# Performance work log

Hardware: AMD Instinct MI355X
Metric: run time of the kernel (lower is better)

The kernel has to match this reference:

```python
import jax, jax.numpy as jnp
import numpy as np

B = 65536
D_EMB = 512      # embedding_dim
D_SPD = 1        # speed_dim
D_LAT = 128      # speed_latent_dim
H = 256          # hidden_size
K = 6            # num_branch
D_IN = D_EMB + D_LAT  # 640, branch/speed-head input dim


def _lin(key, din, dout):
    kw, kb = jax.random.split(key)
    W = jax.random.normal(kw, (din, dout), dtype=jnp.float32) * 0.02
    b = jax.random.normal(kb, (dout,), dtype=jnp.float32) * 0.02
    return W, b


def setup_inputs() -> dict:
    key = jax.random.key(0)
    ks = jax.random.split(key, 16)
    embedding = jax.random.normal(ks[0], (B, D_EMB), dtype=jnp.float32)
    speed = jax.random.uniform(ks[1], (B, D_SPD), dtype=jnp.float32)
    command = jax.random.randint(ks[2], (B,), 1, K + 1, dtype=jnp.int32)  # values 1..6
    # speed input MLP: speed_dim -> H -> D_LAT
    Wsi1, bsi1 = _lin(ks[3], D_SPD, H)
    Wsi2, bsi2 = _lin(ks[4], H, D_LAT)
    # speed prediction head: D_IN -> H -> H -> speed_dim
    Wso1, bso1 = _lin(ks[5], D_IN, H)
    Wso2, bso2 = _lin(ks[6], H, H)
    Wso3, bso3 = _lin(ks[7], H, D_SPD)
    # K branch heads, stacked on leading axis: D_IN -> H -> H -> 3, sigmoid
    def _stack(key, din, dout):
        kw, kb = jax.random.split(key)
        W = jax.random.normal(kw, (K, din, dout), dtype=jnp.float32) * 0.02
        b = jax.random.normal(kb, (K, dout), dtype=jnp.float32) * 0.02
        return W, b
    Wb1, bb1 = _stack(ks[8], D_IN, H)
    Wb2, bb2 = _stack(ks[9], H, H)
    Wb3, bb3 = _stack(ks[10], H, 3)
    return dict(embedding=embedding, speed=speed, command=command,
                Wsi1=Wsi1, bsi1=bsi1, Wsi2=Wsi2, bsi2=bsi2,
                Wso1=Wso1, bso1=bso1, Wso2=Wso2, bso2=bso2, Wso3=Wso3, bso3=bso3,
                Wb1=Wb1, bb1=bb1, Wb2=Wb2, bb2=bb2, Wb3=Wb3, bb3=bb3)


def reference(embedding, speed, command,
              Wsi1, bsi1, Wsi2, bsi2,
              Wso1, bso1, Wso2, bso2, Wso3, bso3,
              Wb1, bb1, Wb2, bb2, Wb3, bb3):
    # speed -> latent
    sp = jax.nn.relu(speed @ Wsi1 + bsi1) @ Wsi2 + bsi2          # [B, D_LAT]
    emb = jnp.concatenate([embedding, sp], axis=1)               # [B, D_IN]
    # compute ALL K branch heads (as the original does), then mask by command
    h = jax.nn.relu(jnp.einsum('bd,kdh->bkh', emb, Wb1) + bb1)   # [B, K, H]
    h = jax.nn.relu(jnp.einsum('bkh,khj->bkj', h, Wb2) + bb2)    # [B, K, H]
    ctrl_all = jax.nn.sigmoid(jnp.einsum('bkh,kho->bko', h, Wb3) + bb3)  # [B, K, 3]
    mask = (command[:, None] - 1 == jnp.arange(K)[None, :]).astype(ctrl_all.dtype)  # [B, K]
    control_pred = jnp.sum(ctrl_all * mask[:, :, None], axis=1)  # [B, 3]
    # speed prediction head
    hs = jax.nn.relu(emb @ Wso1 + bso1)
    hs = jax.nn.relu(hs @ Wso2 + bso2)
    speed_pred = hs @ Wso3 + bso3                                # [B, 1]
    return control_pred, speed_pred
```

## Files before the change

kernel.cpp:

```cpp
#include <hip/hip_runtime.h>
#include <hip/hip_bf16.h>


#define NB 65536
#define NBRB 1030

typedef __attribute__((ext_vector_type(8))) short short8;
typedef __attribute__((ext_vector_type(4))) float f32x4;
typedef unsigned short bhalf;
typedef unsigned int u32;

__device__ __forceinline__ bhalf f2b(float x) {
    __hip_bfloat16 h = __float2bfloat16(x);
    return *reinterpret_cast<bhalf*>(&h);
}
__device__ __forceinline__ void gll16(const void* g, void* l) {
    __builtin_amdgcn_global_load_lds(
        (const __attribute__((address_space(1))) u32*)g,
        (__attribute__((address_space(3))) u32*)l, 16, 0, 0);
}
__device__ __forceinline__ int sadr(int row, int cb) {
    return row * 64 + (cb ^ (((row >> 1) & 3) << 4));
}
__device__ __forceinline__ int yadr(int row, int cb) {
    return row * 512 + (cb ^ ((row & 7) << 4));
}
__device__ __forceinline__ void wvm6() { asm volatile("s_waitcnt vmcnt(6)" ::: "memory"); }
__device__ __forceinline__ void wvm0() { asm volatile("s_waitcnt vmcnt(0)" ::: "memory"); }
__device__ __forceinline__ void wlgkm0() { asm volatile("s_waitcnt lgkmcnt(0)" ::: "memory"); }

__global__ __launch_bounds__(256) void k_wprep(
    const float* __restrict__ Wsi2, const float* __restrict__ Wso1,
    const float* __restrict__ Wso2, const float* __restrict__ Wb1,
    const float* __restrict__ Wb2,
    bhalf* __restrict__ Wsi2T, bhalf* __restrict__ Wso1T,
    bhalf* __restrict__ Wso2T, bhalf* __restrict__ Wb1T,
    bhalf* __restrict__ Wb2T) {
    __shared__ float T[64][65];
    const int id = blockIdx.x, t = threadIdx.x;
    const float* src; bhalf* dst; int K, N, tk, tn, b;
    if (id < 8)        { src = Wsi2; dst = Wsi2T; K = 256; N = 128; b = 0; int tl = id;      tk = tl / 2; tn = tl % 2; }
    else if (id < 48)  { src = Wso1; dst = Wso1T; K = 640; N = 256; b = 0; int tl = id - 8;  tk = tl / 4; tn = tl % 4; }
    else if (id < 64)  { src = Wso2; dst = Wso2T; K = 256; N = 256; b = 0; int tl = id - 48; tk = tl / 4; tn = tl % 4; }
    else if (id < 304) { src = Wb1;  dst = Wb1T;  K = 640; N = 256; int li = id - 64;  b = li / 40; int tl = li % 40; tk = tl / 4; tn = tl % 4; }
    else               { src = Wb2;  dst = Wb2T;  K = 256; N = 256; int li = id - 304; b = li / 16; int tl = li % 16; tk = tl / 4; tn = tl % 4; }
    const int k0 = tk * 64, n0 = tn * 64;
    src += (size_t)b * K * N; dst += (size_t)b * N * K;
    const int c = t & 63, r0 = t >> 6;
#pragma unroll
    for (int j = 0; j < 16; ++j) {
        int r = r0 + j * 4;
        T[r][c] = src[(size_t)(k0 + r) * N + n0 + c];
    }
    __syncthreads();
#pragma unroll
    for (int j = 0; j < 16; ++j) {
        int r = r0 + j * 4;
        dst[(size_t)(n0 + r) * K + k0 + c] = f2b(T[c][r]);
    }
}

__global__ __launch_bounds__(256) void k_prep(
    const float* __restrict__ speed, const float* __restrict__ Wsi1,
    const float* __restrict__ bsi1, const bhalf* __restrict__ Wsi2T,
    const float* __restrict__ bsi2, const int* __restrict__ cmd,
    bhalf* __restrict__ spb, int* __restrict__ bcnt) {
    __shared__ bhalf A[64 * 72];
    __shared__ bhalf BT[128 * 72];
    const int t = threadIdx.x, lane = t & 63, wid = t >> 6;
    const int rbase = blockIdx.x * 64;
    if (wid == 0) {
        int c = cmd[rbase + lane] - 1;
        int v = 0;
#pragma unroll
        for (int g = 0; g < 6; ++g) {
            unsigned long long m = __ballot(c == g);
            if (lane == g) v = (int)__popcll(m);
        }
        if (lane < 6) bcnt[blockIdx.x * 6 + lane] = v;
    }
    const int wm = wid >> 1, wn = wid & 1;
    f32x4 acc[2][4];
    for (int m = 0; m < 2; ++m) for (int n = 0; n < 4; ++n)
        for (int r = 0; r < 4; ++r) acc[m][n][r] = 0.f;
    const int ar = t >> 2, kp = (t & 3) * 16;
    const float s = speed[rbase + ar];
    for (int kc = 0; kc < 4; ++kc) {
        short8 w0, w1;
#pragma unroll
        for (int j = 0; j < 8; ++j) {
            int k = kc * 64 + kp + j;
            w0[j] = (short)f2b(fmaxf(fmaf(s, Wsi1[k], bsi1[k]), 0.f));
            w1[j] = (short)f2b(fmaxf(fmaf(s, Wsi1[k + 8], bsi1[k + 8]), 0.f));
        }
        *(short8*)&A[ar * 72 + kp] = w0;
        *(short8*)&A[ar * 72 + kp + 8] = w1;
#pragma unroll
        for (int j = 0; j < 4; ++j) {
            int ch = t + j * 256;
            int n2 = ch >> 3, ko = (ch & 7) * 8;
            *(short8*)&BT[n2 * 72 + ko] =
                *(const short8*)(Wsi2T + n2 * 256 + kc * 64 + ko);
        }
        __syncthreads();
#pragma unroll
        for (int ks = 0; ks < 2; ++ks) {
            short8 a[2], b[4];
#pragma unroll
            for (int m = 0; m < 2; ++m)
                a[m] = *(const short8*)&A[(wm * 32 + m * 16 + (lane & 15)) * 72 + ks * 32 + (lane >> 4) * 8];
#pragma unroll
            for (int n = 0; n < 4; ++n)
                b[n] = *(const short8*)&BT[(wn * 64 + n * 16 + (lane & 15)) * 72 + ks * 32 + (lane >> 4) * 8];
#pragma unroll
            for (int m = 0; m < 2; ++m)
#pragma unroll
                for (int n = 0; n < 4; ++n)
                    acc[m][n] = __builtin_amdgcn_mfma_f32_16x16x32_bf16(a[m], b[n], acc[m][n], 0, 0, 0);
        }
        __syncthreads();
    }
#pragma unroll
    for (int m = 0; m < 2; ++m)
#pragma unroll
    for (int n = 0; n < 4; ++n) {
        int col = wn * 64 + n * 16 + (lane & 15);
        float bias = bsi2[col];
#pragma unroll
        for (int r = 0; r < 4; ++r) {
            int row = rbase + wm * 32 + m * 16 + (lane >> 4) * 4 + r;
            spb[row * 128 + col] = f2b(acc[m][n][r] + bias);
        }
    }
}

__global__ __launch_bounds__(1024) void k_scan(
    const int* __restrict__ bcnt, int* __restrict__ chunkoff,
    int* __restrict__ pad) {
    __shared__ int sc[1024];
    __shared__ int tot[8];
    __shared__ int spo[8];
    const int t = threadIdx.x;
    for (int g = 0; g < 6; ++g) {
        int v = bcnt[t * 6 + g];
        sc[t] = v;
        __syncthreads();
        for (int s = 1; s < 1024; s <<= 1) {
            int u = (t >= s) ? sc[t - s] : 0;
            __syncthreads();
            sc[t] += u;
            __syncthreads();
        }
        if (t == 1023) tot[g] = sc[t];
        chunkoff[t * 6 + g] = sc[t] - v;
        __syncthreads();
    }
    if (t == 0) {
        int off = 0;
        for (int g = 0; g < 6; ++g) {
            spo[g] = off; pad[g] = off; pad[8 + g] = tot[g];
            off += ((tot[g] + 63) >> 6) << 6;
        }
        spo[6] = off; pad[6] = off;
    }
    __syncthreads();
    for (int g = 0; g < 6; ++g) chunkoff[t * 6 + g] += spo[g];
}

__global__ __launch_bounds__(256) void k_scatter(
    const int* __restrict__ cmd, const int* __restrict__ chunkoff,
    int* __restrict__ perm) {
    const int lane = threadIdx.x & 63, w = threadIdx.x >> 6;
    const int chunk = blockIdx.x * 4 + w;
    const int idx = chunk * 64 + lane;
    const int c = cmd[idx] - 1;
#pragma unroll
    for (int g = 0; g < 6; ++g) {
        unsigned long long m = __ballot(c == g);
        if (c == g) {
            int pos = chunkoff[chunk * 6 + g] + (int)__popcll(m & ((1ull << lane) - 1ull));
            perm[pos] = idx;
        }
    }
}

__global__ __launch_bounds__(256, 3) void k_head(
    const float* __restrict__ emb, const bhalf* __restrict__ spb,
    const bhalf* __restrict__ Wso1T, const float* __restrict__ bso1,
    const bhalf* __restrict__ Wso2T, const float* __restrict__ bso2,
    const float* __restrict__ Wso3, const float* __restrict__ bso3,
    const bhalf* __restrict__ Wb1T, const float* __restrict__ bb1,
    const bhalf* __restrict__ Wb2T, const float* __restrict__ bb2,
    const float* __restrict__ Wb3, const float* __restrict__ bb3,
    const int* __restrict__ pad, const int* __restrict__ perm,
    float* __restrict__ out) {
    __shared__ __align__(16) char L[49152];
    char* const SB0 = L;
    char* const SAr = L + 32768;
    char* const Yb  = L;
    const int t = threadIdx.x, lane = t & 63, wid = t >> 6;
    const bool isB = blockIdx.x < NBRB;
    int tstart, DOUT, gcnt, gbase;
    const bhalf *W1T, *W2T; const float *b1, *b2, *W3, *b3;
    if (isB) {
        tstart = blockIdx.x * 64;
        if (tstart >= pad[6]) return;
        int g = 0;
        while (pad[g + 1] <= tstart) ++g;
        gbase = pad[g]; gcnt = pad[8 + g];
        W1T = Wb1T + (size_t)g * (256 * 640); b1 = bb1 + g * 256;
        W2T = Wb2T + (size_t)g * (256 * 256); b2 = bb2 + g * 256;
        W3  = Wb3  + (size_t)g * (256 * 3);   b3 = bb3 + g * 3;
        DOUT = 3;
    } else {
        tstart = (blockIdx.x - NBRB) * 64;
        gbase = 0; gcnt = NB;
        W1T = Wso1T; b1 = bso1; W2T = Wso2T; b2 = bso2; W3 = Wso3; b3 = bso3;
        DOUT = 1;
    }

    const int rowA0 = t >> 3, rowA1 = rowA0 + 32, rowS = t >> 2;
    int ra0, ra1, raS;
    if (isB) {
        int p0 = tstart + rowA0, p1 = tstart + rowA1, pS = tstart + rowS;
        ra0 = ((p0 - gbase) < gcnt) ? perm[p0] : 0;
        ra1 = ((p1 - gbase) < gcnt) ? perm[p1] : 0;
        raS = ((pS - gbase) < gcnt) ? perm[pS] : 0;
    } else {
        ra0 = tstart + rowA0; ra1 = tstart + rowA1; raS = tstart + rowS;
    }
    const int lcA0 = ((t & 7) * 16) ^ ((rowA0 & 7) << 4);
    const int lcA1 = ((t & 7) * 16) ^ ((rowA1 & 7) << 4);
    const int lcS  = ((t & 3) * 16) ^ (((rowS >> 1) & 3) << 4);
    const char* embp0 = (const char*)(emb + (size_t)ra0 * 512);
    const char* embp1 = (const char*)(emb + (size_t)ra1 * 512);
    const char* spbp  = (const char*)(spb + (size_t)raS * 128);
    const int dstA = t * 16;
    const int rB = t >> 2, cB = (t & 3) * 16;

#define ST_A(KN, BUF) do { int kn_ = (KN); char* d_ = SAr + (BUF) * 8192 + dstA; \
        if (kn_ < 16) {                                                           \
            gll16(embp0 + kn_ * 128 + lcA0, d_);                                  \
            gll16(embp1 + kn_ * 128 + lcA1, d_ + 4096);                           \
        } else {                                                                  \
            gll16(spbp + (kn_ - 16) * 64 + lcS, d_);                              \
            gll16(spbp + (kn_ - 16) * 64 + lcS, d_ + 4096);                       \
        } } while (0)
#define ST_B1(KN, BUF) do {                                                       \
        _Pragma("unroll")                                                         \
        for (int j_ = 0; j_ < 4; ++j_) {                                          \
            int row_ = rB + j_ * 64;                                              \
            int p_ = row_ * 64 + cB;                                              \
            int lc_ = cB ^ (((row_ >> 1) & 3) << 4);                              \
            gll16((const char*)W1T + (size_t)row_ * 1280 + (KN) * 64 + lc_,       \
                  SB0 + (BUF) * 16384 + p_);                                      \
        } } while (0)
#define ST_B2(KB) do {                                                            \
        _Pragma("unroll")                                                         \
        for (int j_ = 0; j_ < 4; ++j_) {                                          \
            int row_ = rB + j_ * 64;                                              \
            int p_ = row_ * 64 + cB;                                              \
            int lc_ = cB ^ (((row_ >> 1) & 3) << 4);                              \
            gll16((const char*)W2T + (size_t)row_ * 512 + (KB) + lc_,             \
                  SAr + p_);                                                      \
        } } while (0)

    const int arow = lane & 15, koff = (lane >> 4) * 16;
    float bi1[4], bi2[4];
#pragma unroll
    for (int n = 0; n < 4; ++n) {
        bi1[n] = b1[wid * 64 + n * 16 + arow];
        bi2[n] = b2[wid * 64 + n * 16 + arow];
    }

    f32x4 acc[4][4];
#pragma unroll
    for (int m = 0; m < 4; ++m)
#pragma unroll
        for (int n = 0; n < 4; ++n)
#pragma unroll
            for (int r = 0; r < 4; ++r) acc[m][n][r] = 0.f;

    ST_A(0, 0); ST_B1(0, 0);
    for (int kc = 0; kc < 20; ++kc) {
        const int buf = kc & 1;
        if (kc < 19) { ST_A(kc + 1, buf ^ 1); ST_B1(kc + 1, buf ^ 1); wvm6(); }
        else         { wvm0(); }
        __builtin_amdgcn_s_barrier();
        const char* SAc = SAr + buf * 8192;
        const char* SBc = SB0 + buf * 16384;
        short8 a[4], b[4];
#pragma unroll
        for (int n = 0; n < 4; ++n)
            b[n] = *(const short8*)(SBc + sadr(wid * 64 + n * 16 + arow, koff));
        if (kc < 16) {
#pragma unroll
            for (int m = 0; m < 4; ++m) {
                int row = m * 16 + arow;
                int sw = (row & 7) << 4;
                int c0 = (lane >> 4) * 32;
                float4 f0 = *(const float4*)(SAc + row * 128 + (c0 ^ sw));
                float4 f1 = *(const float4*)(SAc + row * 128 + ((c0 + 16) ^ sw));
                a[m][0] = (short)f2b(f0.x); a[m][1] = (short)f2b(f0.y);
                a[m][2] = (short)f2b(f0.z); a[m][3] = (short)f2b(f0.w);
                a[m][4] = (short)f2b(f1.x); a[m][5] = (short)f2b(f1.y);
                a[m][6] = (short)f2b(f1.z); a[m][7] = (short)f2b(f1.w);
            }
        } else {
#pragma unroll
            for (int m = 0; m < 4; ++m)
                a[m] = *(const short8*)(SAc + sadr(m * 16 + arow, koff));
        }
#pragma unroll
        for (int m = 0; m < 4; ++m)
#pragma unroll
            for (int n = 0; n < 4; ++n)
                acc[m][n] = __builtin_amdgcn_mfma_f32_16x16x32_bf16(a[m], b[n], acc[m][n], 0, 0, 0);
        __builtin_amdgcn_s_barrier();
    }
#pragma unroll
    for (int m = 0; m < 4; ++m)
#pragma unroll
    for (int n = 0; n < 4; ++n) {
        int col = wid * 64 + n * 16 + arow;
#pragma unroll
        for (int r = 0; r < 4; ++r) {
            int row = m * 16 + (lane >> 4) * 4 + r;
            *(bhalf*)(Yb + yadr(row, 2 * col)) = f2b(fmaxf(acc[m][n][r] + bi1[n], 0.f));
            acc[m][n][r] = 0.f;
        }
    }
    ST_B2(0);
    wlgkm0();
    wvm0();
    __builtin_amdgcn_s_barrier();
    for (int kc = 0; kc < 8; ++kc) {
        short8 a[4], b[4];
#pragma unroll
        for (int m = 0; m < 4; ++m)
            a[m] = *(const short8*)(Yb + yadr(m * 16 + arow, kc * 64 + koff));
#pragma unroll
        for (int n = 0; n < 4; ++n)
            b[n] = *(const short8*)(SAr + sadr(wid * 64 + n * 16 + arow, koff));
#pragma unroll
        for (int m = 0; m < 4; ++m)
#pragma unroll
            for (int n = 0; n < 4; ++n)
                acc[m][n] = __builtin_amdgcn_mfma_f32_16x16x32_bf16(a[m], b[n], acc[m][n], 0, 0, 0);
        __builtin_amdgcn_s_barrier();
        if (kc < 7) { ST_B2((kc + 1) * 64); wvm0(); }
        __builtin_amdgcn_s_barrier();
    }
#pragma unroll
    for (int m = 0; m < 4; ++m)
#pragma unroll
    for (int n = 0; n < 4; ++n) {
        int col = wid * 64 + n * 16 + arow;
#pragma unroll
        for (int r = 0; r < 4; ++r) {
            int row = m * 16 + (lane >> 4) * 4 + r;
            *(bhalf*)(Yb + yadr(row, 2 * col)) = f2b(fmaxf(acc[m][n][r] + bi2[n], 0.f));
        }
    }
    wlgkm0();
    __builtin_amdgcn_s_barrier();
    f32x4 z;
#pragma unroll
    for (int r = 0; r < 4; ++r) z[r] = 0.f;
    const int col3 = arow;
    for (int kc = 0; kc < 8; ++kc) {
        short8 a3 = *(const short8*)(Yb + yadr(wid * 16 + arow, kc * 64 + koff));
        short8 bw;
#pragma unroll
        for (int j = 0; j < 8; ++j) bw[j] = 0;
        if (col3 < DOUT) {
            int kb = kc * 32 + (lane >> 4) * 8;
#pragma unroll
            for (int j = 0; j < 8; ++j)
                bw[j] = (short)f2b(W3[(kb + j) * DOUT + col3]);
        }
        z = __builtin_amdgcn_mfma_f32_16x16x32_bf16(a3, bw, z, 0, 0, 0);
    }
    if (col3 < DOUT) {
        float bias = b3[col3];
#pragma unroll
        for (int rr = 0; rr < 4; ++rr) {
            int r = wid * 16 + (lane >> 4) * 4 + rr;
            int p2 = tstart + r;
            if ((p2 - gbase) < gcnt) {
                float v = z[rr] + bias;
                if (isB) {
                    int ro = perm[p2];
                    out[(size_t)ro * 3 + col3] = 1.f / (1.f + __expf(-v));
                } else {
                    out[(size_t)NB * 3 + p2] = v;
                }
            }
        }
    }
#undef ST_A
#undef ST_B1
#undef ST_B2
}

extern "C" void kernel_launch(void* const* d_in, const int* in_sizes, int n_in,
                              void* d_out, int out_size, void* d_ws, size_t ws_size,
                              hipStream_t stream) {
    (void)in_sizes; (void)n_in; (void)out_size; (void)ws_size;
    const float* emb   = (const float*)d_in[0];
    const float* speed = (const float*)d_in[1];
    const int*   cmd   = (const int*)d_in[2];
    const float* Wsi1  = (const float*)d_in[3];
    const float* bsi1  = (const float*)d_in[4];
    const float* Wsi2  = (const float*)d_in[5];
    const float* bsi2  = (const float*)d_in[6];
    const float* Wso1  = (const float*)d_in[7];
    const float* bso1  = (const float*)d_in[8];
    const float* Wso2  = (const float*)d_in[9];
    const float* bso2  = (const float*)d_in[10];
    const float* Wso3  = (const float*)d_in[11];
    const float* bso3  = (const float*)d_in[12];
    const float* Wb1   = (const float*)d_in[13];
    const float* bb1   = (const float*)d_in[14];
    const float* Wb2   = (const float*)d_in[15];
    const float* bb2   = (const float*)d_in[16];
    const float* Wb3   = (const float*)d_in[17];
    const float* bb3   = (const float*)d_in[18];
    float* out = (float*)d_out;

    char* ws = (char*)d_ws;
    bhalf* spb      = (bhalf*)(ws);
    int*   perm     = (int*)(ws + 16777216);
    int*   bcnt     = (int*)(ws + 17040896);
    int*   chunkoff = (int*)(ws + 17065472);
    int*   pad      = (int*)(ws + 17090048);
    bhalf* Wsi2T    = (bhalf*)(ws + 17090304);
    bhalf* Wso1T    = (bhalf*)(ws + 17155840);
    bhalf* Wso2T    = (bhalf*)(ws + 17483520);
    bhalf* Wb1T     = (bhalf*)(ws + 17614592);
    bhalf* Wb2T     = (bhalf*)(ws + 19580672);

    k_wprep<<<400, 256, 0, stream>>>(Wsi2, Wso1, Wso2, Wb1, Wb2,
                                     Wsi2T, Wso1T, Wso2T, Wb1T, Wb2T);
    k_prep<<<NB / 64, 256, 0, stream>>>(speed, Wsi1, bsi1, Wsi2T, bsi2, cmd,
                                        spb, bcnt);
    k_scan<<<1, 1024, 0, stream>>>(bcnt, chunkoff, pad);
    k_scatter<<<NB / 256, 256, 0, stream>>>(cmd, chunkoff, perm);
    k_head<<<NBRB + NB / 64, 256, 0, stream>>>(emb, spb,
                                               Wso1T, bso1, Wso2T, bso2, Wso3, bso3,
                                               Wb1T, bb1, Wb2T, bb2, Wb3, bb3,
                                               pad, perm, out);
}
```

Before: 155.7 us.

## Load MLP weight fragments directly from global into registers, bypassing LDS staging

Both hidden-layer GEMMs now read their weight operand per wave straight from global memory into registers, instead of staging weight tiles cooperatively in LDS. This drops the W1/W2 LDS copies, the LDS reads for the B operand, and the double barrier in the second-layer loop. Shared memory is split into an activation double buffer and the Y buffer. The cost is that each weight fetch is issued at the start of its iteration without prefetch, so global/L2 latency sits on the critical path unless occupancy hides it. Weight reads are also less coalesced: each row gives only 64-byte contiguous segments with a large stride.

```diff
diff --git a/kernel.cpp b/kernel.cpp
--- a/kernel.cpp
+++ b/kernel.cpp
@@ -26,7 +26,7 @@
     return row * 512 + (cb ^ ((row & 7) << 4));
 }
 __device__ __forceinline__ void wvm6() { asm volatile("s_waitcnt vmcnt(6)" ::: "memory"); }
-__device__ __forceinline__ void wvm0() { asm volatile("s_waitcnt vmcnt(0)" ::: "memory"); }
+__device__ __forceinline__ void wvm4() { asm volatile("s_waitcnt vmcnt(4)" ::: "memory"); }
 __device__ __forceinline__ void wlgkm0() { asm volatile("s_waitcnt lgkmcnt(0)" ::: "memory"); }
 
 __global__ __launch_bounds__(256) void k_wprep(
@@ -194,10 +194,8 @@
     const float* __restrict__ Wb3, const float* __restrict__ bb3,
     const int* __restrict__ pad, const int* __restrict__ perm,
     float* __restrict__ out) {
-    __shared__ __align__(16) char L[49152];
-    char* const SB0 = L;
-    char* const SAr = L + 32768;
-    char* const Yb  = L;
+    __shared__ __align__(16) char SA[2][8192];
+    __shared__ __align__(16) char Yb[32768];
     const int t = threadIdx.x, lane = t & 63, wid = t >> 6;
     const bool isB = blockIdx.x < NBRB;
     int tstart, DOUT, gcnt, gbase;
@@ -236,9 +234,8 @@
     const char* embp1 = (const char*)(emb + (size_t)ra1 * 512);
     const char* spbp  = (const char*)(spb + (size_t)raS * 128);
     const int dstA = t * 16;
-    const int rB = t >> 2, cB = (t & 3) * 16;
-
-#define ST_A(KN, BUF) do { int kn_ = (KN); char* d_ = SAr + (BUF) * 8192 + dstA; \
+
+#define ST_A(KN, BUF) do { int kn_ = (KN); char* d_ = &SA[BUF][0] + dstA;        \
         if (kn_ < 16) {                                                           \
             gll16(embp0 + kn_ * 128 + lcA0, d_);                                  \
             gll16(embp1 + kn_ * 128 + lcA1, d_ + 4096);                           \
@@ -246,26 +243,14 @@
             gll16(spbp + (kn_ - 16) * 64 + lcS, d_);                              \
             gll16(spbp + (kn_ - 16) * 64 + lcS, d_ + 4096);                       \
         } } while (0)
-#define ST_B1(KN, BUF) do {                                                       \
-        _Pragma("unroll")                                                         \
-        for (int j_ = 0; j_ < 4; ++j_) {                                          \
-            int row_ = rB + j_ * 64;                                              \
-            int p_ = row_ * 64 + cB;                                              \
-            int lc_ = cB ^ (((row_ >> 1) & 3) << 4);                              \
-            gll16((const char*)W1T + (size_t)row_ * 1280 + (KN) * 64 + lc_,       \
-                  SB0 + (BUF) * 16384 + p_);                                      \
-        } } while (0)
-#define ST_B2(KB) do {                                                            \
-        _Pragma("unroll")                                                         \
-        for (int j_ = 0; j_ < 4; ++j_) {                                          \
-            int row_ = rB + j_ * 64;                                              \
-            int p_ = row_ * 64 + cB;                                              \
-            int lc_ = cB ^ (((row_ >> 1) & 3) << 4);                              \
-            gll16((const char*)W2T + (size_t)row_ * 512 + (KB) + lc_,             \
-                  SAr + p_);                                                      \
-        } } while (0)
 
     const int arow = lane & 15, koff = (lane >> 4) * 16;
+    const int kb = (lane >> 4) * 16;
+    const char* bp0 = (const char*)W1T + (size_t)(wid * 64 + 0  + arow) * 1280 + kb;
+    const char* bp1 = (const char*)W1T + (size_t)(wid * 64 + 16 + arow) * 1280 + kb;
+    const char* bp2 = (const char*)W1T + (size_t)(wid * 64 + 32 + arow) * 1280 + kb;
+    const char* bp3 = (const char*)W1T + (size_t)(wid * 64 + 48 + arow) * 1280 + kb;
+
     float bi1[4], bi2[4];
 #pragma unroll
     for (int n = 0; n < 4; ++n) {
@@ -281,18 +266,18 @@
 #pragma unroll
             for (int r = 0; r < 4; ++r) acc[m][n][r] = 0.f;
 
-    ST_A(0, 0); ST_B1(0, 0);
+    ST_A(0, 0);
     for (int kc = 0; kc < 20; ++kc) {
         const int buf = kc & 1;
-        if (kc < 19) { ST_A(kc + 1, buf ^ 1); ST_B1(kc + 1, buf ^ 1); wvm6(); }
-        else         { wvm0(); }
+        short8 b0 = *(const short8*)(bp0 + kc * 64);
+        short8 b1f = *(const short8*)(bp1 + kc * 64);
+        short8 b2f = *(const short8*)(bp2 + kc * 64);
+        short8 b3f = *(const short8*)(bp3 + kc * 64);
+        if (kc < 19) { ST_A(kc + 1, buf ^ 1); wvm6(); }
+        else         { wvm4(); }
         __builtin_amdgcn_s_barrier();
-        const char* SAc = SAr + buf * 8192;
-        const char* SBc = SB0 + buf * 16384;
-        short8 a[4], b[4];
-#pragma unroll
-        for (int n = 0; n < 4; ++n)
-            b[n] = *(const short8*)(SBc + sadr(wid * 64 + n * 16 + arow, koff));
+        const char* SAc = &SA[buf][0];
+        short8 a[4];
         if (kc < 16) {
 #pragma unroll
             for (int m = 0; m < 4; ++m) {
@@ -312,10 +297,12 @@
                 a[m] = *(const short8*)(SAc + sadr(m * 16 + arow, koff));
         }
 #pragma unroll
-        for (int m = 0; m < 4; ++m)
-#pragma unroll
-            for (int n = 0; n < 4; ++n)
-                acc[m][n] = __builtin_amdgcn_mfma_f32_16x16x32_bf16(a[m], b[n], acc[m][n], 0, 0, 0);
+        for (int m = 0; m < 4; ++m) {
+            acc[m][0] = __builtin_amdgcn_mfma_f32_16x16x32_bf16(a[m], b0,  acc[m][0], 0, 0, 0);
+            acc[m][1] = __builtin_amdgcn_mfma_f32_16x16x32_bf16(a[m], b1f, acc[m][1], 0, 0, 0);
+            acc[m][2] = __builtin_amdgcn_mfma_f32_16x16x32_bf16(a[m], b2f, acc[m][2], 0, 0, 0);
+            acc[m][3] = __builtin_amdgcn_mfma_f32_16x16x32_bf16(a[m], b3f, acc[m][3], 0, 0, 0);
+        }
         __builtin_amdgcn_s_barrier();
     }
 #pragma unroll
@@ -330,27 +317,32 @@
             acc[m][n][r] = 0.f;
         }
     }
-    ST_B2(0);
     wlgkm0();
-    wvm0();
     __builtin_amdgcn_s_barrier();
-    for (int kc = 0; kc < 8; ++kc) {
-        short8 a[4], b[4];
-#pragma unroll
-        for (int m = 0; m < 4; ++m)
-            a[m] = *(const short8*)(Yb + yadr(m * 16 + arow, kc * 64 + koff));
-#pragma unroll
-        for (int n = 0; n < 4; ++n)
-            b[n] = *(const short8*)(SAr + sadr(wid * 64 + n * 16 + arow, koff));
-#pragma unroll
-        for (int m = 0; m < 4; ++m)
-#pragma unroll
-            for (int n = 0; n < 4; ++n)
-                acc[m][n] = __builtin_amdgcn_mfma_f32_16x16x32_bf16(a[m], b[n], acc[m][n], 0, 0, 0);
-        __builtin_amdgcn_s_barrier();
-        if (kc < 7) { ST_B2((kc + 1) * 64); wvm0(); }
-        __builtin_amdgcn_s_barrier();
-    }
+    {
+        const char* cp0 = (const char*)W2T + (size_t)(wid * 64 + 0  + arow) * 512 + kb;
+        const char* cp1 = (const char*)W2T + (size_t)(wid * 64 + 16 + arow) * 512 + kb;
+        const char* cp2 = (const char*)W2T + (size_t)(wid * 64 + 32 + arow) * 512 + kb;
+        const char* cp3 = (const char*)W2T + (size_t)(wid * 64 + 48 + arow) * 512 + kb;
+        for (int kc = 0; kc < 8; ++kc) {
+            short8 b0 = *(const short8*)(cp0 + kc * 64);
+            short8 b1f = *(const short8*)(cp1 + kc * 64);
+            short8 b2f = *(const short8*)(cp2 + kc * 64);
+            short8 b3f = *(const short8*)(cp3 + kc * 64);
+            short8 a[4];
+#pragma unroll
+            for (int m = 0; m < 4; ++m)
+                a[m] = *(const short8*)(Yb + yadr(m * 16 + arow, kc * 64 + koff));
+#pragma unroll
+            for (int m = 0; m < 4; ++m) {
+                acc[m][0] = __builtin_amdgcn_mfma_f32_16x16x32_bf16(a[m], b0,  acc[m][0], 0, 0, 0);
+                acc[m][1] = __builtin_amdgcn_mfma_f32_16x16x32_bf16(a[m], b1f, acc[m][1], 0, 0, 0);
+                acc[m][2] = __builtin_amdgcn_mfma_f32_16x16x32_bf16(a[m], b2f, acc[m][2], 0, 0, 0);
+                acc[m][3] = __builtin_amdgcn_mfma_f32_16x16x32_bf16(a[m], b3f, acc[m][3], 0, 0, 0);
+            }
+        }
+    }
+    __builtin_amdgcn_s_barrier();
 #pragma unroll
     for (int m = 0; m < 4; ++m)
 #pragma unroll
@@ -374,10 +366,10 @@
 #pragma unroll
         for (int j = 0; j < 8; ++j) bw[j] = 0;
         if (col3 < DOUT) {
-            int kb = kc * 32 + (lane >> 4) * 8;
+            int kbq = kc * 32 + (lane >> 4) * 8;
 #pragma unroll
             for (int j = 0; j < 8; ++j)
-                bw[j] = (short)f2b(W3[(kb + j) * DOUT + col3]);
+                bw[j] = (short)f2b(W3[(kbq + j) * DOUT + col3]);
         }
         z = __builtin_amdgcn_mfma_f32_16x16x32_bf16(a3, bw, z, 0, 0, 0);
     }
@@ -399,8 +391,6 @@
         }
     }
 #undef ST_A
-#undef ST_B1
-#undef ST_B2
 }
 
 extern "C" void kernel_launch(void* const* d_in, const int* in_sizes, int n_in,
```

After: 184.6 us. 1.19x slower.

## Share gathered embedding tile between branch and speed heads via two-stage kernels

Applied to the files above, without the earlier changes.

Replaces the single k_head launch, which used separate blocks for branch rows and speed rows, with two kernels over the command-sorted row tiles. Each block computes both the selected branch layer and the speed-head layer for the same 64 rows, so the embedding is loaded and converted once instead of twice. The first-layer activations are written to a bf16 workspace buffer and read back by a second kernel, which applies layer 2 and layer 3 for both heads. The cost is an extra global round trip for the intermediate (64K x 1 KB), larger LDS and register use per block that lowers occupancy, and a fallback path to k_head when the workspace is too small.

```diff
diff --git a/kernel.cpp b/kernel.cpp
--- a/kernel.cpp
+++ b/kernel.cpp
@@ -4,6 +4,8 @@
 
 #define NB 65536
 #define NBRB 1030
+#define NG2 1032
+#define WS_NEED 88000256ULL
 
 typedef __attribute__((ext_vector_type(8))) short short8;
 typedef __attribute__((ext_vector_type(4))) float f32x4;
@@ -25,9 +27,13 @@
 __device__ __forceinline__ int yadr(int row, int cb) {
     return row * 512 + (cb ^ ((row & 7) << 4));
 }
-__device__ __forceinline__ void wvm6() { asm volatile("s_waitcnt vmcnt(6)" ::: "memory"); }
-__device__ __forceinline__ void wvm0() { asm volatile("s_waitcnt vmcnt(0)" ::: "memory"); }
-__device__ __forceinline__ void wlgkm0() { asm volatile("s_waitcnt lgkmcnt(0)" ::: "memory"); }
+__device__ __forceinline__ int yadr2(int row, int cb) {
+    return row * 1024 + (cb ^ ((row & 7) << 4));
+}
+__device__ __forceinline__ void wvm10() { asm volatile("s_waitcnt vmcnt(10)" ::: "memory"); }
+__device__ __forceinline__ void wvm6()  { asm volatile("s_waitcnt vmcnt(6)"  ::: "memory"); }
+__device__ __forceinline__ void wvm0()  { asm volatile("s_waitcnt vmcnt(0)"  ::: "memory"); }
+__device__ __forceinline__ void wlgkm0(){ asm volatile("s_waitcnt lgkmcnt(0)" ::: "memory"); }
 
 __global__ __launch_bounds__(256) void k_wprep(
     const float* __restrict__ Wsi2, const float* __restrict__ Wso1,
@@ -182,6 +188,282 @@
             perm[pos] = idx;
         }
     }
+}
+
+__global__ __launch_bounds__(256, 2) void k1(
+    const float* __restrict__ emb, const bhalf* __restrict__ spb,
+    const bhalf* __restrict__ Wso1T, const float* __restrict__ bso1,
+    const bhalf* __restrict__ Wb1T, const float* __restrict__ bb1,
+    const int* __restrict__ pad, const int* __restrict__ perm,
+    bhalf* __restrict__ Yg) {
+    __shared__ __align__(16) char L[81920];
+    char* const SA0 = L;
+    char* const SB0 = L + 16384;
+    const int t = threadIdx.x, lane = t & 63, wid = t >> 6;
+    const int tstart = blockIdx.x * 64;
+    if (tstart >= pad[6]) return;
+    int g = 0;
+    while (pad[g + 1] <= tstart) ++g;
+    const int gbase = pad[g], gcnt = pad[8 + g];
+    const bhalf* W1b = Wb1T + (size_t)g * (256 * 640);
+
+    const int rowA0 = t >> 3, rowA1 = rowA0 + 32, rowS = t >> 2;
+    int p0 = tstart + rowA0, p1 = tstart + rowA1, pS = tstart + rowS;
+    const int ra0 = ((p0 - gbase) < gcnt) ? perm[p0] : 0;
+    const int ra1 = ((p1 - gbase) < gcnt) ? perm[p1] : 0;
+    const int raS = ((pS - gbase) < gcnt) ? perm[pS] : 0;
+    const int lcA0 = ((t & 7) * 16) ^ ((rowA0 & 7) << 4);
+    const int lcA1 = ((t & 7) * 16) ^ ((rowA1 & 7) << 4);
+    const int lcS  = ((t & 3) * 16) ^ (((rowS >> 1) & 3) << 4);
+    const char* embp0 = (const char*)(emb + (size_t)ra0 * 512);
+    const char* embp1 = (const char*)(emb + (size_t)ra1 * 512);
+    const char* spbp  = (const char*)(spb + (size_t)raS * 128);
+    const int dstA = t * 16;
+    const int rB = t >> 2, cB = (t & 3) * 16;
+
+#define ST_A(KN, BUF) do { int kn_ = (KN); char* d_ = SA0 + (BUF) * 8192 + dstA; \
+        if (kn_ < 16) {                                                           \
+            gll16(embp0 + kn_ * 128 + lcA0, d_);                                  \
+            gll16(embp1 + kn_ * 128 + lcA1, d_ + 4096);                           \
+        } else {                                                                  \
+            gll16(spbp + (kn_ - 16) * 64 + lcS, d_);                              \
+            gll16(spbp + (kn_ - 16) * 64 + lcS, d_ + 4096);                       \
+        } } while (0)
+#define ST_B(KN, BUF) do {                                                        \
+        _Pragma("unroll")                                                         \
+        for (int j_ = 0; j_ < 4; ++j_) {                                          \
+            int row_ = rB + j_ * 64;                                              \
+            int p_ = row_ * 64 + cB;                                              \
+            int lc_ = cB ^ (((row_ >> 1) & 3) << 4);                              \
+            gll16((const char*)W1b + (size_t)row_ * 1280 + (KN) * 64 + lc_,       \
+                  SB0 + (BUF) * 32768 + p_);                                      \
+            gll16((const char*)Wso1T + (size_t)row_ * 1280 + (KN) * 64 + lc_,     \
+                  SB0 + (BUF) * 32768 + 16384 + p_);                              \
+        } } while (0)
+
+    const int arow = lane & 15, koff = (lane >> 4) * 16;
+    float bi1[8];
+#pragma unroll
+    for (int n = 0; n < 4; ++n) {
+        bi1[n]     = bb1[g * 256 + wid * 64 + n * 16 + arow];
+        bi1[n + 4] = bso1[wid * 64 + n * 16 + arow];
+    }
+
+    f32x4 acc[4][8];
+#pragma unroll
+    for (int m = 0; m < 4; ++m)
+#pragma unroll
+        for (int n = 0; n < 8; ++n)
+#pragma unroll
+            for (int r = 0; r < 4; ++r) acc[m][n][r] = 0.f;
+
+    ST_A(0, 0); ST_B(0, 0);
+    for (int kc = 0; kc < 20; ++kc) {
+        const int buf = kc & 1;
+        if (kc < 19) { ST_A(kc + 1, buf ^ 1); ST_B(kc + 1, buf ^ 1); wvm10(); }
+        else         { wvm0(); }
+        __builtin_amdgcn_s_barrier();
+        const char* SAc = SA0 + buf * 8192;
+        const char* SBc = SB0 + buf * 32768;
+        short8 a[4], b[8];
+#pragma unroll
+        for (int n = 0; n < 4; ++n) {
+            b[n]     = *(const short8*)(SBc + sadr(wid * 64 + n * 16 + arow, koff));
+            b[n + 4] = *(const short8*)(SBc + 16384 + sadr(wid * 64 + n * 16 + arow, koff));
+        }
+        if (kc < 16) {
+#pragma unroll
+            for (int m = 0; m < 4; ++m) {
+                int row = m * 16 + arow;
+                int sw = (row & 7) << 4;
+                int c0 = (lane >> 4) * 32;
+                float4 f0 = *(const float4*)(SAc + row * 128 + (c0 ^ sw));
+                float4 f1 = *(const float4*)(SAc + row * 128 + ((c0 + 16) ^ sw));
+                a[m][0] = (short)f2b(f0.x); a[m][1] = (short)f2b(f0.y);
+                a[m][2] = (short)f2b(f0.z); a[m][3] = (short)f2b(f0.w);
+                a[m][4] = (short)f2b(f1.x); a[m][5] = (short)f2b(f1.y);
+                a[m][6] = (short)f2b(f1.z); a[m][7] = (short)f2b(f1.w);
+            }
+        } else {
+#pragma unroll
+            for (int m = 0; m < 4; ++m)
+                a[m] = *(const short8*)(SAc + sadr(m * 16 + arow, koff));
+        }
+#pragma unroll
+        for (int m = 0; m < 4; ++m)
+#pragma unroll
+            for (int n = 0; n < 8; ++n)
+                acc[m][n] = __builtin_amdgcn_mfma_f32_16x16x32_bf16(a[m], b[n], acc[m][n], 0, 0, 0);
+        __builtin_amdgcn_s_barrier();
+    }
+#pragma unroll
+    for (int m = 0; m < 4; ++m)
+#pragma unroll
+    for (int n = 0; n < 8; ++n) {
+        int col = (n < 4) ? (wid * 64 + n * 16 + arow)
+                          : (256 + wid * 64 + (n - 4) * 16 + arow);
+#pragma unroll
+        for (int r = 0; r < 4; ++r) {
+            int row = m * 16 + (lane >> 4) * 4 + r;
+            *(bhalf*)(L + yadr2(row, 2 * col)) = f2b(fmaxf(acc[m][n][r] + bi1[n], 0.f));
+        }
+    }
+    wlgkm0();
+    __builtin_amdgcn_s_barrier();
+    char* Ygb = (char*)Yg + (size_t)tstart * 1024;
+#pragma unroll
+    for (int j = 0; j < 16; ++j) {
+        int p = t * 16 + j * 4096;
+        int row = p >> 10, cb = p & 1023;
+        uint4 v = *(const uint4*)(L + row * 1024 + (cb ^ ((row & 7) << 4)));
+        *(uint4*)(Ygb + (size_t)row * 1024 + cb) = v;
+    }
+#undef ST_A
+#undef ST_B
+}
+
+__global__ __launch_bounds__(256, 2) void k2(
+    const bhalf* __restrict__ Yg,
+    const bhalf* __restrict__ Wso2T, const float* __restrict__ bso2,
+    const float* __restrict__ Wso3, const float* __restrict__ bso3,
+    const bhalf* __restrict__ Wb2T, const float* __restrict__ bb2,
+    const float* __restrict__ Wb3, const float* __restrict__ bb3,
+    const int* __restrict__ pad, const int* __restrict__ perm,
+    float* __restrict__ out) {
+    __shared__ __align__(16) char L[81920];
+    char* const SA0 = L;
+    char* const SB0 = L + 16384;
+    const int t = threadIdx.x, lane = t & 63, wid = t >> 6;
+    const int tstart = blockIdx.x * 64;
+    if (tstart >= pad[6]) return;
+    int g = 0;
+    while (pad[g + 1] <= tstart) ++g;
+    const int gbase = pad[g], gcnt = pad[8 + g];
+    const bhalf* W2b = Wb2T + (size_t)g * (256 * 256);
+    const float* W3b = Wb3 + (size_t)g * (256 * 3);
+    const float* b3b = bb3 + g * 3;
+
+    const int rowY = t >> 2, cA = (t & 3) * 16;
+    const int lcA = cA ^ (((rowY >> 1) & 3) << 4);
+    const char* ygp = (const char*)Yg + (size_t)(tstart + rowY) * 1024;
+    const int dstA = t * 16;
+    const int rB = t >> 2, cB = (t & 3) * 16;
+
+#define ST_A2(KC, BUF) do { char* d_ = SA0 + (BUF) * 8192 + dstA;                \
+        gll16(ygp + (KC) * 64 + lcA, d_);                                         \
+        gll16(ygp + 512 + (KC) * 64 + lcA, d_ + 4096);                            \
+    } while (0)
+#define ST_B2(KC, BUF) do {                                                       \
+        _Pragma("unroll")                                                         \
+        for (int j_ = 0; j_ < 4; ++j_) {                                          \
+            int row_ = rB + j_ * 64;                                              \
+            int p_ = row_ * 64 + cB;                                              \
+            int lc_ = cB ^ (((row_ >> 1) & 3) << 4);                              \
+            gll16((const char*)W2b + (size_t)row_ * 512 + (KC) * 64 + lc_,        \
+                  SB0 + (BUF) * 32768 + p_);                                      \
+            gll16((const char*)Wso2T + (size_t)row_ * 512 + (KC) * 64 + lc_,      \
+                  SB0 + (BUF) * 32768 + 16384 + p_);                              \
+        } } while (0)
+
+    const int arow = lane & 15, koff = (lane >> 4) * 16;
+    float bi2[8];
+#pragma unroll
+    for (int n = 0; n < 4; ++n) {
+        bi2[n]     = bb2[g * 256 + wid * 64 + n * 16 + arow];
+        bi2[n + 4] = bso2[wid * 64 + n * 16 + arow];
+    }
+
+    f32x4 acc[4][8];
+#pragma unroll
+    for (int m = 0; m < 4; ++m)
+#pragma unroll
+        for (int n = 0; n < 8; ++n)
+#pragma unroll
+            for (int r = 0; r < 4; ++r) acc[m][n][r] = 0.f;
+
+    ST_A2(0, 0); ST_B2(0, 0);
+    for (int kc = 0; kc < 8; ++kc) {
+        const int buf = kc & 1;
+        if (kc < 7) { ST_A2(kc + 1, buf ^ 1); ST_B2(kc + 1, buf ^ 1); wvm10(); }
+        else        { wvm0(); }
+        __builtin_amdgcn_s_barrier();
+        const char* SAc = SA0 + buf * 8192;
+        const char* SBc = SB0 + buf * 32768;
+        short8 aB[4], aS[4], b[8];
+#pragma unroll
+        for (int m = 0; m < 4; ++m) {
+            aB[m] = *(const short8*)(SAc + sadr(m * 16 + arow, koff));
+            aS[m] = *(const short8*)(SAc + 4096 + sadr(m * 16 + arow, koff));
+        }
+#pragma unroll
+        for (int n = 0; n < 4; ++n) {
+            b[n]     = *(const short8*)(SBc + sadr(wid * 64 + n * 16 + arow, koff));
+            b[n + 4] = *(const short8*)(SBc + 16384 + sadr(wid * 64 + n * 16 + arow, koff));
+        }
+#pragma unroll
+        for (int m = 0; m < 4; ++m)
+#pragma unroll
+            for (int n = 0; n < 4; ++n) {
+                acc[m][n]     = __builtin_amdgcn_mfma_f32_16x16x32_bf16(aB[m], b[n],     acc[m][n],     0, 0, 0);
+                acc[m][n + 4] = __builtin_amdgcn_mfma_f32_16x16x32_bf16(aS[m], b[n + 4], acc[m][n + 4], 0, 0, 0);
+            }
+        __builtin_amdgcn_s_barrier();
+    }
+#pragma unroll
+    for (int m = 0; m < 4; ++m)
+#pragma unroll
+    for (int n = 0; n < 8; ++n) {
+        int col = (n < 4) ? (wid * 64 + n * 16 + arow)
+                          : (256 + wid * 64 + (n - 4) * 16 + arow);
+#pragma unroll
+        for (int r = 0; r < 4; ++r) {
+            int row = m * 16 + (lane >> 4) * 4 + r;
+            *(bhalf*)(L + yadr2(row, 2 * col)) = f2b(fmaxf(acc[m][n][r] + bi2[n], 0.f));
+        }
+    }
+    wlgkm0();
+    __builtin_amdgcn_s_barrier();
+    f32x4 zB, zS;
+#pragma unroll
+    for (int r = 0; r < 4; ++r) { zB[r] = 0.f; zS[r] = 0.f; }
+    const int col3 = arow;
+    for (int kc = 0; kc < 8; ++kc) {
+        short8 a3b = *(const short8*)(L + yadr2(wid * 16 + arow, kc * 64 + koff));
+        short8 a3s = *(const short8*)(L + yadr2(wid * 16 + arow, 512 + kc * 64 + koff));
+        short8 bwB, bwS;
+#pragma unroll
+        for (int j = 0; j < 8; ++j) { bwB[j] = 0; bwS[j] = 0; }
+        int kb = kc * 32 + (lane >> 4) * 8;
+        if (col3 < 3) {
+#pragma unroll
+            for (int j = 0; j < 8; ++j)
+                bwB[j] = (short)f2b(W3b[(kb + j) * 3 + col3]);
+        }
+        if (col3 < 1) {
+#pragma unroll
+            for (int j = 0; j < 8; ++j)
+                bwS[j] = (short)f2b(Wso3[kb + j]);
+        }
+        zB = __builtin_amdgcn_mfma_f32_16x16x32_bf16(a3b, bwB, zB, 0, 0, 0);
+        zS = __builtin_amdgcn_mfma_f32_16x16x32_bf16(a3s, bwS, zS, 0, 0, 0);
+    }
+#pragma unroll
+    for (int rr = 0; rr < 4; ++rr) {
+        int r = wid * 16 + (lane >> 4) * 4 + rr;
+        int p2 = tstart + r;
+        if ((p2 - gbase) < gcnt) {
+            int ro = perm[p2];
+            if (col3 < 3) {
+                float v = zB[rr] + b3b[col3];
+                out[(size_t)ro * 3 + col3] = 1.f / (1.f + __expf(-v));
+            }
+            if (col3 < 1) {
+                out[(size_t)NB * 3 + ro] = zS[rr] + bso3[0];
+            }
+        }
+    }
+#undef ST_A2
+#undef ST_B2
 }
 
 __global__ __launch_bounds__(256, 3) void k_head(
@@ -218,7 +500,6 @@
         W1T = Wso1T; b1 = bso1; W2T = Wso2T; b2 = bso2; W3 = Wso3; b3 = bso3;
         DOUT = 1;
     }
-
     const int rowA0 = t >> 3, rowA1 = rowA0 + 32, rowS = t >> 2;
     int ra0, ra1, raS;
     if (isB) {
@@ -237,7 +518,6 @@
     const char* spbp  = (const char*)(spb + (size_t)raS * 128);
     const int dstA = t * 16;
     const int rB = t >> 2, cB = (t & 3) * 16;
-
 #define ST_A(KN, BUF) do { int kn_ = (KN); char* d_ = SAr + (BUF) * 8192 + dstA; \
         if (kn_ < 16) {                                                           \
             gll16(embp0 + kn_ * 128 + lcA0, d_);                                  \
@@ -264,7 +544,6 @@
             gll16((const char*)W2T + (size_t)row_ * 512 + (KB) + lc_,             \
                   SAr + p_);                                                      \
         } } while (0)
-
     const int arow = lane & 15, koff = (lane >> 4) * 16;
     float bi1[4], bi2[4];
 #pragma unroll
@@ -272,7 +551,6 @@
         bi1[n] = b1[wid * 64 + n * 16 + arow];
         bi2[n] = b2[wid * 64 + n * 16 + arow];
     }
-
     f32x4 acc[4][4];
 #pragma unroll
     for (int m = 0; m < 4; ++m)
@@ -280,7 +558,6 @@
         for (int n = 0; n < 4; ++n)
 #pragma unroll
             for (int r = 0; r < 4; ++r) acc[m][n][r] = 0.f;
-
     ST_A(0, 0); ST_B1(0, 0);
     for (int kc = 0; kc < 20; ++kc) {
         const int buf = kc & 1;
@@ -374,10 +651,10 @@
 #pragma unroll
         for (int j = 0; j < 8; ++j) bw[j] = 0;
         if (col3 < DOUT) {
-            int kb = kc * 32 + (lane >> 4) * 8;
+            int kbq = kc * 32 + (lane >> 4) * 8;
 #pragma unroll
             for (int j = 0; j < 8; ++j)
-                bw[j] = (short)f2b(W3[(kb + j) * DOUT + col3]);
+                bw[j] = (short)f2b(W3[(kbq + j) * DOUT + col3]);
         }
         z = __builtin_amdgcn_mfma_f32_16x16x32_bf16(a3, bw, z, 0, 0, 0);
     }
@@ -406,7 +683,7 @@
 extern "C" void kernel_launch(void* const* d_in, const int* in_sizes, int n_in,
                               void* d_out, int out_size, void* d_ws, size_t ws_size,
                               hipStream_t stream) {
-    (void)in_sizes; (void)n_in; (void)out_size; (void)ws_size;
+    (void)in_sizes; (void)n_in; (void)out_size;
     const float* emb   = (const float*)d_in[0];
     const float* speed = (const float*)d_in[1];
     const int*   cmd   = (const int*)d_in[2];
@@ -439,6 +716,7 @@
     bhalf* Wso2T    = (bhalf*)(ws + 17483520);
     bhalf* Wb1T     = (bhalf*)(ws + 17614592);
     bhalf* Wb2T     = (bhalf*)(ws + 19580672);
+    bhalf* Yg       = (bhalf*)(ws + 20367104);
 
     k_wprep<<<400, 256, 0, stream>>>(Wsi2, Wso1, Wso2, Wb1, Wb2,
                                      Wsi2T, Wso1T, Wso2T, Wb1T, Wb2T);
@@ -446,8 +724,15 @@
                                         spb, bcnt);
     k_scan<<<1, 1024, 0, stream>>>(bcnt, chunkoff, pad);
     k_scatter<<<NB / 256, 256, 0, stream>>>(cmd, chunkoff, perm);
-    k_head<<<NBRB + NB / 64, 256, 0, stream>>>(emb, spb,
-                                               Wso1T, bso1, Wso2T, bso2, Wso3, bso3,
-                                               Wb1T, bb1, Wb2T, bb2, Wb3, bb3,
-                                               pad, perm, out);
-}
+    if (ws_size >= WS_NEED) {
+        k1<<<NG2, 256, 0, stream>>>(emb, spb, Wso1T, bso1, Wb1T, bb1,
+                                    pad, perm, Yg);
+        k2<<<NG2, 256, 0, stream>>>(Yg, Wso2T, bso2, Wso3, bso3,
+                                    Wb2T, bb2, Wb3, bb3, pad, perm, out);
+    } else {
+        k_head<<<NBRB + NB / 64, 256, 0, stream>>>(emb, spb,
+                                                   Wso1T, bso1, Wso2T, bso2, Wso3, bso3,
+                                                   Wb1T, bb1, Wb2T, bb2, Wb3, bb3,
+                                                   pad, perm, out);
+    }
+}
```

After: 178.9 us. 1.15x slower.
